# Kernel tuning notes

Measured on AMD Instinct MI355X. Metric: run time of the kernel, lower is better.

Reference implementation:

```python
import jax, jax.numpy as jnp
import numpy as np

T = 16384       # video length (frames)
C = 7           # out_features = d_model = num surgical phases
F_DIM = 2048    # mstcn_f_dim (spatial feature dim)
LEN_Q = 30      # sliding window length
N_HEADS = 4
D_K = 64        # attn_dim = min(64, mstcn_f_maps=64)
D_FF = 64       # d_ff = mstcn_f_maps


def setup_inputs() -> dict:
    key = jax.random.key(0)
    ks = jax.random.split(key, 10)
    w = lambda i, shape: jax.random.normal(ks[i], shape, jnp.float32) * 0.05
    return {
        "x": jax.random.normal(ks[0], (1, C, T), jnp.float32),
        "long_feature": jax.random.normal(ks[1], (1, T, F_DIM), jnp.float32),
        "W_fc": w(2, (C, F_DIM)),              # nn.Linear(mstcn_f_dim, out_features, bias=False)
        "W_q": w(3, (N_HEADS * D_K, C)),
        "W_k": w(4, (N_HEADS * D_K, C)),
        "W_v": w(5, (N_HEADS * D_K, C)),
        "W_o": w(6, (C, N_HEADS * D_K)),
        "ln1_g": jnp.ones((C,), jnp.float32),
        "ln1_b": jnp.zeros((C,), jnp.float32),
        "W_ff1": w(7, (D_FF, C)),
        "W_ff2": w(8, (C, D_FF)),
        "ln2_g": jnp.ones((C,), jnp.float32),
        "ln2_b": jnp.zeros((C,), jnp.float32),
    }


def layer_norm(x, g, b, eps=1e-5):
    mu = x.mean(-1, keepdims=True)
    var = ((x - mu) ** 2).mean(-1, keepdims=True)
    return (x - mu) * jax.lax.rsqrt(var + eps) * g + b


def reference(x, long_feature, W_fc, W_q, W_k, W_v, W_o, ln1_g, ln1_b, W_ff1, W_ff2, ln2_g, ln2_b):
    # --- vectorized sliding-window (replaces the Python loop of zeros/cat/stack) ---
    feats = x[0].T                                            # (T, C)
    padded = jnp.concatenate([jnp.zeros((LEN_Q - 1, C), feats.dtype), feats], axis=0)
    idx = jnp.arange(T)[:, None] + jnp.arange(LEN_Q)[None, :]  # window ends at frame i
    inputs = padded[idx]                                       # (T, LEN_Q, C)

    # --- spatial embedding: feas = tanh(fc(long_feature)).transpose(0,1) ---
    feas = jnp.tanh(long_feature[0] @ W_fc.T)[:, None, :]      # (T, 1, C)

    # --- decoder layer: cross MHA(query=feas, kv=inputs) + residual + LN ---
    q = (feas @ W_q.T).reshape(T, 1, N_HEADS, D_K).transpose(0, 2, 1, 3)       # (T,H,1,Dk)
    k = (inputs @ W_k.T).reshape(T, LEN_Q, N_HEADS, D_K).transpose(0, 2, 1, 3)  # (T,H,Lq,Dk)
    v = (inputs @ W_v.T).reshape(T, LEN_Q, N_HEADS, D_K).transpose(0, 2, 1, 3)  # (T,H,Lq,Dk)
    scores = jnp.einsum('thqd,thkd->thqk', q, k) / np.float32(np.sqrt(D_K))
    attn = jax.nn.softmax(scores, axis=-1)
    ctx = jnp.einsum('thqk,thkd->thqd', attn, v)
    ctx = ctx.transpose(0, 2, 1, 3).reshape(T, 1, N_HEADS * D_K)
    out = layer_norm(ctx @ W_o.T + feas, ln1_g, ln1_b)         # (T, 1, C)

    # --- position-wise FFN + residual + LN ---
    ff = jax.nn.relu(out @ W_ff1.T) @ W_ff2.T
    out = layer_norm(ff + out, ln2_g, ln2_b)
    return out[:, 0]                                           # (T, C) per-frame logits
```

## Files before the change

kernel.cpp:

```cpp
#include <hip/hip_runtime.h>
#include <math.h>

#define T_FRAMES 16384
#define FDIM 2048
#define LQ 30

__global__ __launch_bounds__(448) void setup_kernel(
    const float* __restrict__ Wq, const float* __restrict__ Wk,
    const float* __restrict__ Wv, const float* __restrict__ Wo,
    float* __restrict__ AM) {
  const int e = threadIdx.x;
  if (e >= 392) return;
  const int which = e / 196;
  const int r = e % 196;
  const int h = r / 49;
  const int rr = r % 49;
  const int c = rr / 7;
  const int c2 = rr % 7;
  float s = 0.0f;
  if (which == 0) {
    for (int d = 0; d < 64; ++d)
      s = fmaf(Wq[(h * 64 + d) * 7 + c], Wk[(h * 64 + d) * 7 + c2], s);
  } else {
    for (int d = 0; d < 64; ++d)
      s = fmaf(Wo[c * 256 + h * 64 + d], Wv[(h * 64 + d) * 7 + c2], s);
  }
  AM[e] = s;
}

__global__ __launch_bounds__(256) void feas_kernel(
    const float* __restrict__ lf, const float* __restrict__ Wfc,
    float* __restrict__ feas) {
  const int lane = threadIdx.x & 63;
  const int wave = threadIdx.x >> 6;
  const int t0 = blockIdx.x * 16 + wave * 4;
  const float* lfp = lf + (size_t)t0 * FDIM;

  float acc[4][7];
#pragma unroll
  for (int fr = 0; fr < 4; ++fr)
#pragma unroll
    for (int c = 0; c < 7; ++c) acc[fr][c] = 0.0f;

  for (int chunk = 0; chunk < 8; ++chunk) {
    const int f = chunk * 256 + lane * 4;
    const float4 a0 = *(const float4*)(lfp + 0 * FDIM + f);
    const float4 a1 = *(const float4*)(lfp + 1 * FDIM + f);
    const float4 a2 = *(const float4*)(lfp + 2 * FDIM + f);
    const float4 a3 = *(const float4*)(lfp + 3 * FDIM + f);
#pragma unroll
    for (int c = 0; c < 7; ++c) {
      const float4 w = *(const float4*)(Wfc + c * FDIM + f);
      acc[0][c] = fmaf(a0.x, w.x, fmaf(a0.y, w.y, fmaf(a0.z, w.z, fmaf(a0.w, w.w, acc[0][c]))));
      acc[1][c] = fmaf(a1.x, w.x, fmaf(a1.y, w.y, fmaf(a1.z, w.z, fmaf(a1.w, w.w, acc[1][c]))));
      acc[2][c] = fmaf(a2.x, w.x, fmaf(a2.y, w.y, fmaf(a2.z, w.z, fmaf(a2.w, w.w, acc[2][c]))));
      acc[3][c] = fmaf(a3.x, w.x, fmaf(a3.y, w.y, fmaf(a3.z, w.z, fmaf(a3.w, w.w, acc[3][c]))));
    }
  }

#pragma unroll
  for (int fr = 0; fr < 4; ++fr) {
#pragma unroll
    for (int c = 0; c < 7; ++c) {
      float v = acc[fr][c];
      for (int off = 32; off > 0; off >>= 1) v += __shfl_down(v, off, 64);
      if (lane == 0) feas[(size_t)(t0 + fr) * 7 + c] = tanhf(v);
    }
  }
}

__global__ __launch_bounds__(64) void attn_kernel(
    const float* __restrict__ x,
    const float* __restrict__ feas,
    const float* __restrict__ AM,
    const float* __restrict__ W1,
    const float* __restrict__ W2,
    const float* __restrict__ ln1g, const float* __restrict__ ln1b,
    const float* __restrict__ ln2g, const float* __restrict__ ln2b,
    float* __restrict__ out) {
  __shared__ float ft[93 * 7];
  const int t0 = blockIdx.x * 64;
  const int tid = threadIdx.x;

  for (int c = 0; c < 7; ++c) {
    for (int i = tid; i < 93; i += 64) {
      const int s = t0 - 29 + i;
      ft[i * 7 + c] = (s >= 0) ? x[c * T_FRAMES + s] : 0.0f;
    }
  }
  __syncthreads();

  const int t = t0 + tid;
  float fe[7];
#pragma unroll
  for (int c = 0; c < 7; ++c) fe[c] = feas[(size_t)t * 7 + c];

  const float* frow = &ft[tid * 7];
  float outp[7] = {0, 0, 0, 0, 0, 0, 0};

#pragma unroll
  for (int h = 0; h < 4; ++h) {
    const float* Ah = AM + h * 49;
    const float* Mh = AM + 196 + h * 49;
    float qk[7];
#pragma unroll
    for (int c2 = 0; c2 < 7; ++c2) {
      float s = 0.0f;
#pragma unroll
      for (int c = 0; c < 7; ++c) s = fmaf(fe[c], Ah[c * 7 + c2], s);
      qk[c2] = s * 0.125f;
    }
    float sc[LQ];
    float m = -1e30f;
#pragma unroll
    for (int j = 0; j < LQ; ++j) {
      const float* r = frow + j * 7;
      float s = 0.0f;
#pragma unroll
      for (int c2 = 0; c2 < 7; ++c2) s = fmaf(qk[c2], r[c2], s);
      sc[j] = s;
      m = fmaxf(m, s);
    }
    float sum = 0.0f;
    float wsum[7] = {0, 0, 0, 0, 0, 0, 0};
#pragma unroll
    for (int j = 0; j < LQ; ++j) {
      const float p = __expf(sc[j] - m);
      sum += p;
      const float* r = frow + j * 7;
#pragma unroll
      for (int c2 = 0; c2 < 7; ++c2) wsum[c2] = fmaf(p, r[c2], wsum[c2]);
    }
    const float inv = 1.0f / sum;
#pragma unroll
    for (int c = 0; c < 7; ++c) {
      float s = 0.0f;
#pragma unroll
      for (int c2 = 0; c2 < 7; ++c2) s = fmaf(Mh[c * 7 + c2], wsum[c2], s);
      outp[c] = fmaf(s, inv, outp[c]);
    }
  }

  float v[7];
#pragma unroll
  for (int c = 0; c < 7; ++c) v[c] = outp[c] + fe[c];
  float mu = 0.0f;
#pragma unroll
  for (int c = 0; c < 7; ++c) mu += v[c];
  mu *= (1.0f / 7.0f);
  float var = 0.0f;
#pragma unroll
  for (int c = 0; c < 7; ++c) { const float d = v[c] - mu; var = fmaf(d, d, var); }
  var *= (1.0f / 7.0f);
  float rs = rsqrtf(var + 1e-5f);
  float o1[7];
#pragma unroll
  for (int c = 0; c < 7; ++c) o1[c] = (v[c] - mu) * rs * ln1g[c] + ln1b[c];

  float ff[7] = {0, 0, 0, 0, 0, 0, 0};
  for (int k = 0; k < 64; ++k) {
    float hk = 0.0f;
#pragma unroll
    for (int c = 0; c < 7; ++c) hk = fmaf(W1[k * 7 + c], o1[c], hk);
    hk = fmaxf(hk, 0.0f);
#pragma unroll
    for (int c = 0; c < 7; ++c) ff[c] = fmaf(W2[c * 64 + k], hk, ff[c]);
  }

#pragma unroll
  for (int c = 0; c < 7; ++c) v[c] = ff[c] + o1[c];
  mu = 0.0f;
#pragma unroll
  for (int c = 0; c < 7; ++c) mu += v[c];
  mu *= (1.0f / 7.0f);
  var = 0.0f;
#pragma unroll
  for (int c = 0; c < 7; ++c) { const float d = v[c] - mu; var = fmaf(d, d, var); }
  var *= (1.0f / 7.0f);
  rs = rsqrtf(var + 1e-5f);
#pragma unroll
  for (int c = 0; c < 7; ++c)
    out[(size_t)t * 7 + c] = (v[c] - mu) * rs * ln2g[c] + ln2b[c];
}

extern "C" void kernel_launch(void* const* d_in, const int* in_sizes, int n_in,
                              void* d_out, int out_size, void* d_ws, size_t ws_size,
                              hipStream_t stream) {
  const float* x    = (const float*)d_in[0];
  const float* lf   = (const float*)d_in[1];
  const float* Wfc  = (const float*)d_in[2];
  const float* Wq   = (const float*)d_in[3];
  const float* Wk   = (const float*)d_in[4];
  const float* Wv   = (const float*)d_in[5];
  const float* Wo   = (const float*)d_in[6];
  const float* ln1g = (const float*)d_in[7];
  const float* ln1b = (const float*)d_in[8];
  const float* W1   = (const float*)d_in[9];
  const float* W2   = (const float*)d_in[10];
  const float* ln2g = (const float*)d_in[11];
  const float* ln2b = (const float*)d_in[12];
  float* out = (float*)d_out;

  float* feas = (float*)d_ws;
  float* AM   = feas + (size_t)T_FRAMES * 7;

  setup_kernel<<<1, 448, 0, stream>>>(Wq, Wk, Wv, Wo, AM);
  feas_kernel<<<T_FRAMES / 16, 256, 0, stream>>>(lf, Wfc, feas);
  attn_kernel<<<T_FRAMES / 64, 64, 0, stream>>>(x, feas, AM, W1, W2,
                                                ln1g, ln1b, ln2g, ln2b, out);
}
```

Baseline: 260.1 us.

## Fuse feature projection and attention into one kernel with per-head threads

Merges the long-feature projection kernel and the attention/FFN kernel into a single launch. The tanh-projected features stay in shared memory instead of going through a global workspace, and attention is spread across threads, one per frame-head pair, with head partials reduced in shared memory. This removes a kernel launch and the feas round trip, and gives the attention stage more parallelism. In exchange, the FFN/LayerNorm tail runs on only 16 threads per block, and the x window plus AM are reloaded per 16-frame block.

```diff
diff --git a/kernel.cpp b/kernel.cpp
--- a/kernel.cpp
+++ b/kernel.cpp
@@ -4,6 +4,7 @@
 #define T_FRAMES 16384
 #define FDIM 2048
 #define LQ 30
+#define FPB 16
 
 __global__ __launch_bounds__(448) void setup_kernel(
     const float* __restrict__ Wq, const float* __restrict__ Wk,
@@ -28,14 +29,35 @@
   AM[e] = s;
 }
 
-__global__ __launch_bounds__(256) void feas_kernel(
-    const float* __restrict__ lf, const float* __restrict__ Wfc,
-    float* __restrict__ feas) {
-  const int lane = threadIdx.x & 63;
-  const int wave = threadIdx.x >> 6;
-  const int t0 = blockIdx.x * 16 + wave * 4;
-  const float* lfp = lf + (size_t)t0 * FDIM;
-
+__global__ __launch_bounds__(256) void fused_kernel(
+    const float* __restrict__ lf,
+    const float* __restrict__ Wfc,
+    const float* __restrict__ x,
+    const float* __restrict__ AM,
+    const float* __restrict__ W1,
+    const float* __restrict__ W2,
+    const float* __restrict__ ln1g, const float* __restrict__ ln1b,
+    const float* __restrict__ ln2g, const float* __restrict__ ln2b,
+    float* __restrict__ out) {
+  __shared__ float feas_s[FPB][7];
+  __shared__ float AM_s[392];
+  __shared__ float ft[(FPB + LQ - 1) * 7];
+  __shared__ float hpart[FPB][4][7];
+
+  const int tid = threadIdx.x;
+  const int lane = tid & 63;
+  const int wave = tid >> 6;
+  const int t0 = blockIdx.x * FPB;
+
+  for (int i = tid; i < 392; i += 256) AM_s[i] = AM[i];
+  for (int i = tid; i < (FPB + LQ - 1) * 7; i += 256) {
+    const int row = i / 7, c = i % 7;
+    const int s = t0 - (LQ - 1) + row;
+    ft[i] = (s >= 0) ? x[c * T_FRAMES + s] : 0.0f;
+  }
+
+  const int tf = t0 + wave * 4;
+  const float* lfp = lf + (size_t)tf * FDIM;
   float acc[4][7];
 #pragma unroll
   for (int fr = 0; fr < 4; ++fr)
@@ -64,44 +86,20 @@
     for (int c = 0; c < 7; ++c) {
       float v = acc[fr][c];
       for (int off = 32; off > 0; off >>= 1) v += __shfl_down(v, off, 64);
-      if (lane == 0) feas[(size_t)(t0 + fr) * 7 + c] = tanhf(v);
-    }
-  }
-}
-
-__global__ __launch_bounds__(64) void attn_kernel(
-    const float* __restrict__ x,
-    const float* __restrict__ feas,
-    const float* __restrict__ AM,
-    const float* __restrict__ W1,
-    const float* __restrict__ W2,
-    const float* __restrict__ ln1g, const float* __restrict__ ln1b,
-    const float* __restrict__ ln2g, const float* __restrict__ ln2b,
-    float* __restrict__ out) {
-  __shared__ float ft[93 * 7];
-  const int t0 = blockIdx.x * 64;
-  const int tid = threadIdx.x;
-
-  for (int c = 0; c < 7; ++c) {
-    for (int i = tid; i < 93; i += 64) {
-      const int s = t0 - 29 + i;
-      ft[i * 7 + c] = (s >= 0) ? x[c * T_FRAMES + s] : 0.0f;
+      if (lane == 0) feas_s[wave * 4 + fr][c] = tanhf(v);
     }
   }
   __syncthreads();
 
-  const int t = t0 + tid;
-  float fe[7];
-#pragma unroll
-  for (int c = 0; c < 7; ++c) fe[c] = feas[(size_t)t * 7 + c];
-
-  const float* frow = &ft[tid * 7];
-  float outp[7] = {0, 0, 0, 0, 0, 0, 0};
-
-#pragma unroll
-  for (int h = 0; h < 4; ++h) {
-    const float* Ah = AM + h * 49;
-    const float* Mh = AM + 196 + h * 49;
+  if (tid < FPB * 4) {
+    const int f = tid >> 2;
+    const int h = tid & 3;
+    float fe[7];
+#pragma unroll
+    for (int c = 0; c < 7; ++c) fe[c] = feas_s[f][c];
+
+    const float* Ah = AM_s + h * 49;
+    const float* Mh = AM_s + 196 + h * 49;
     float qk[7];
 #pragma unroll
     for (int c2 = 0; c2 < 7; ++c2) {
@@ -110,6 +108,7 @@
       for (int c = 0; c < 7; ++c) s = fmaf(fe[c], Ah[c * 7 + c2], s);
       qk[c2] = s * 0.125f;
     }
+    const float* frow = &ft[f * 7];
     float sc[LQ];
     float m = -1e30f;
 #pragma unroll
@@ -137,50 +136,57 @@
       float s = 0.0f;
 #pragma unroll
       for (int c2 = 0; c2 < 7; ++c2) s = fmaf(Mh[c * 7 + c2], wsum[c2], s);
-      outp[c] = fmaf(s, inv, outp[c]);
-    }
-  }
-
-  float v[7];
-#pragma unroll
-  for (int c = 0; c < 7; ++c) v[c] = outp[c] + fe[c];
-  float mu = 0.0f;
-#pragma unroll
-  for (int c = 0; c < 7; ++c) mu += v[c];
-  mu *= (1.0f / 7.0f);
-  float var = 0.0f;
-#pragma unroll
-  for (int c = 0; c < 7; ++c) { const float d = v[c] - mu; var = fmaf(d, d, var); }
-  var *= (1.0f / 7.0f);
-  float rs = rsqrtf(var + 1e-5f);
-  float o1[7];
-#pragma unroll
-  for (int c = 0; c < 7; ++c) o1[c] = (v[c] - mu) * rs * ln1g[c] + ln1b[c];
-
-  float ff[7] = {0, 0, 0, 0, 0, 0, 0};
-  for (int k = 0; k < 64; ++k) {
-    float hk = 0.0f;
-#pragma unroll
-    for (int c = 0; c < 7; ++c) hk = fmaf(W1[k * 7 + c], o1[c], hk);
-    hk = fmaxf(hk, 0.0f);
-#pragma unroll
-    for (int c = 0; c < 7; ++c) ff[c] = fmaf(W2[c * 64 + k], hk, ff[c]);
-  }
-
-#pragma unroll
-  for (int c = 0; c < 7; ++c) v[c] = ff[c] + o1[c];
-  mu = 0.0f;
-#pragma unroll
-  for (int c = 0; c < 7; ++c) mu += v[c];
-  mu *= (1.0f / 7.0f);
-  var = 0.0f;
-#pragma unroll
-  for (int c = 0; c < 7; ++c) { const float d = v[c] - mu; var = fmaf(d, d, var); }
-  var *= (1.0f / 7.0f);
-  rs = rsqrtf(var + 1e-5f);
-#pragma unroll
-  for (int c = 0; c < 7; ++c)
-    out[(size_t)t * 7 + c] = (v[c] - mu) * rs * ln2g[c] + ln2b[c];
+      hpart[f][h][c] = s * inv;
+    }
+  }
+  __syncthreads();
+
+  if (tid < FPB) {
+    const int f = tid;
+    float v[7];
+#pragma unroll
+    for (int c = 0; c < 7; ++c)
+      v[c] = feas_s[f][c] + hpart[f][0][c] + hpart[f][1][c] + hpart[f][2][c] + hpart[f][3][c];
+
+    float mu = 0.0f;
+#pragma unroll
+    for (int c = 0; c < 7; ++c) mu += v[c];
+    mu *= (1.0f / 7.0f);
+    float var = 0.0f;
+#pragma unroll
+    for (int c = 0; c < 7; ++c) { const float d = v[c] - mu; var = fmaf(d, d, var); }
+    var *= (1.0f / 7.0f);
+    float rs = rsqrtf(var + 1e-5f);
+    float o1[7];
+#pragma unroll
+    for (int c = 0; c < 7; ++c) o1[c] = (v[c] - mu) * rs * ln1g[c] + ln1b[c];
+
+    float ff[7] = {0, 0, 0, 0, 0, 0, 0};
+    for (int k = 0; k < 64; ++k) {
+      float hk = 0.0f;
+#pragma unroll
+      for (int c = 0; c < 7; ++c) hk = fmaf(W1[k * 7 + c], o1[c], hk);
+      hk = fmaxf(hk, 0.0f);
+#pragma unroll
+      for (int c = 0; c < 7; ++c) ff[c] = fmaf(W2[c * 64 + k], hk, ff[c]);
+    }
+
+#pragma unroll
+    for (int c = 0; c < 7; ++c) v[c] = ff[c] + o1[c];
+    mu = 0.0f;
+#pragma unroll
+    for (int c = 0; c < 7; ++c) mu += v[c];
+    mu *= (1.0f / 7.0f);
+    var = 0.0f;
+#pragma unroll
+    for (int c = 0; c < 7; ++c) { const float d = v[c] - mu; var = fmaf(d, d, var); }
+    var *= (1.0f / 7.0f);
+    rs = rsqrtf(var + 1e-5f);
+    const int t = t0 + f;
+#pragma unroll
+    for (int c = 0; c < 7; ++c)
+      out[(size_t)t * 7 + c] = (v[c] - mu) * rs * ln2g[c] + ln2b[c];
+  }
 }
 
 extern "C" void kernel_launch(void* const* d_in, const int* in_sizes, int n_in,
@@ -201,11 +207,9 @@
   const float* ln2b = (const float*)d_in[12];
   float* out = (float*)d_out;
 
-  float* feas = (float*)d_ws;
-  float* AM   = feas + (size_t)T_FRAMES * 7;
+  float* AM = (float*)d_ws;
 
   setup_kernel<<<1, 448, 0, stream>>>(Wq, Wk, Wv, Wo, AM);
-  feas_kernel<<<T_FRAMES / 16, 256, 0, stream>>>(lf, Wfc, feas);
-  attn_kernel<<<T_FRAMES / 64, 64, 0, stream>>>(x, feas, AM, W1, W2,
-                                                ln1g, ln1b, ln2g, ln2b, out);
+  fused_kernel<<<T_FRAMES / FPB, 256, 0, stream>>>(
+      lf, Wfc, x, AM, W1, W2, ln1g, ln1b, ln2g, ln2b, out);
 }
```

New measurement: 254.3 us. 1.02x faster.
